# Performance work log

Measured on AMD Instinct MI355X. Metric: run time of the kernel, lower is better.

## Reference

```python
import jax, jax.numpy as jnp
import numpy as np

N = 16384
K = 10
NODE_IN, RF_IN, TXP_IN = 8, 64, 64
EMB = 64            # node_output_dim = rf_output_dim = txp_output_dim
HID = 128           # hidden_dim (fusion output)
DGC = 64            # dgcn_dim
NUM_CLS = 16        # num_node_classes


def _linear_params(key, fan_in, fan_out):
    kw, kb = jax.random.split(key)
    lim = 1.0 / np.sqrt(fan_in)
    W = jax.random.uniform(kw, (fan_in, fan_out), minval=-lim, maxval=lim, dtype=jnp.float32)
    b = jax.random.uniform(kb, (fan_out,), minval=-lim, maxval=lim, dtype=jnp.float32)
    return W, b


def setup_inputs() -> dict:
    key = jax.random.key(0)
    ks = jax.random.split(key, 12)
    node_feat = jax.random.normal(ks[0], (N, NODE_IN), dtype=jnp.float32)
    rf_feat = jax.random.normal(ks[1], (N, RF_IN), dtype=jnp.float32)
    txp_feat = jax.random.normal(ks[2], (N, TXP_IN), dtype=jnp.float32)
    Wb, bb = _linear_params(ks[3], NODE_IN, EMB)
    Wr, br = _linear_params(ks[4], RF_IN, EMB)
    Wt, bt = _linear_params(ks[5], TXP_IN, EMB)
    Wf, bf = _linear_params(ks[6], 3 * EMB, HID)
    We1, be1 = _linear_params(ks[7], 2 * HID, DGC)   # EdgeConv 1 MLP
    We2, be2 = _linear_params(ks[8], 2 * DGC, DGC)   # EdgeConv 2 MLP
    Wc, bc = _linear_params(ks[9], 2 * DGC, NUM_CLS)  # node classifier on concat of both conv outputs
    return {"node_feat": node_feat, "rf_feat": rf_feat, "txp_feat": txp_feat,
            "Wb": Wb, "bb": bb, "Wr": Wr, "br": br, "Wt": Wt, "bt": bt,
            "Wf": Wf, "bf": bf, "We1": We1, "be1": be1, "We2": We2, "be2": be2,
            "Wc": Wc, "bc": bc}


def _knn_idx(x, k):
    # pairwise squared euclidean distances, exclude self, k nearest
    sq = jnp.sum(x * x, axis=1)                      # [N]
    d = sq[:, None] + sq[None, :] - 2.0 * (x @ x.T)  # [N, N]
    n = x.shape[0]
    d = d.at[jnp.arange(n), jnp.arange(n)].set(jnp.inf)
    _, idx = jax.lax.top_k(-d, k)                    # [N, k]
    return idx


def _edge_conv(x, W, b, k):
    # dynamic KNN graph + EdgeConv: max_j leaky_relu(MLP([x_i, x_j - x_i]))
    idx = _knn_idx(x, k)                             # [N, k] int
    xj = x[idx]                                      # [N, k, d]  irregular gather
    xi = jnp.broadcast_to(x[:, None, :], xj.shape)
    e = jnp.concatenate([xi, xj - xi], axis=-1)      # [N, k, 2d]
    h = jax.nn.leaky_relu(jnp.einsum('nke,eo->nko', e, W) + b)
    return jnp.max(h, axis=1)                        # [N, out] max aggregation


def reference(node_feat, rf_feat, txp_feat, Wb, bb, Wr, br, Wt, bt,
              Wf, bf, We1, be1, We2, be2, Wc, bc):
    # per-modality embeds (Linear + ReLU)
    xb = jax.nn.relu(node_feat @ Wb + bb)
    xr = jax.nn.relu(rf_feat @ Wr + br)
    xt = jax.nn.relu(txp_feat @ Wt + bt)
    # fusion (Linear + LeakyReLU)
    h = jax.nn.leaky_relu(jnp.concatenate([xb, xr, xt], axis=-1) @ Wf + bf)  # [N, HID]
    # two dynamic-graph conv (DGC) layers with per-layer KNN
    g1 = _edge_conv(h, We1, be1, K)    # [N, DGC]
    g2 = _edge_conv(g1, We2, be2, K)   # [N, DGC]
    # node classifier on concatenated conv outputs
    logits = jnp.concatenate([g1, g2], axis=-1) @ Wc + bc  # [N, NUM_CLS]
    return logits
```

## Files before the change

### kernel.cpp

```cpp
#include <hip/hip_runtime.h>
#include <hip/hip_bf16.h>

#define N_NODES 16384
#define KNBR 10

__device__ __forceinline__ void gload_lds16(const float* g, void* l) {
    __builtin_amdgcn_global_load_lds((const __attribute__((address_space(1))) void*)g,
                                     (__attribute__((address_space(3))) void*)l,
                                     16, 0, 0);
}

__global__ __launch_bounds__(256) void embed_kernel(
        const float* __restrict__ nf, const float* __restrict__ rf,
        const float* __restrict__ tf,
        const float* __restrict__ Wb, const float* __restrict__ bb,
        const float* __restrict__ Wr, const float* __restrict__ br,
        const float* __restrict__ Wt, const float* __restrict__ bt,
        float* __restrict__ xcat, int n) {
    int t = blockIdx.x * blockDim.x + threadIdx.x;
    if (t >= n * 192) return;
    int i = t / 192, o = t % 192;
    float acc;
    if (o < 64) {
        acc = bb[o];
        #pragma unroll
        for (int d = 0; d < 8; ++d) acc = fmaf(nf[i * 8 + d], Wb[d * 64 + o], acc);
    } else if (o < 128) {
        int oo = o - 64;
        acc = br[oo];
        #pragma unroll 8
        for (int d = 0; d < 64; ++d) acc = fmaf(rf[i * 64 + d], Wr[d * 64 + oo], acc);
    } else {
        int oo = o - 128;
        acc = bt[oo];
        #pragma unroll 8
        for (int d = 0; d < 64; ++d) acc = fmaf(tf[i * 64 + d], Wt[d * 64 + oo], acc);
    }
    xcat[t] = fmaxf(acc, 0.0f);
}

__global__ __launch_bounds__(256) void fuse_kernel(
        const float* __restrict__ xcat, const float* __restrict__ Wf,
        const float* __restrict__ bf, float* __restrict__ h, int n) {
    int t = blockIdx.x * blockDim.x + threadIdx.x;
    if (t >= n * 128) return;
    int i = t >> 7, o = t & 127;
    float acc = bf[o];
    const float* xr = xcat + (size_t)i * 192;
    #pragma unroll 8
    for (int d = 0; d < 192; ++d) acc = fmaf(xr[d], Wf[d * 128 + o], acc);
    h[t] = acc > 0.f ? acc : 0.01f * acc;
}

__global__ void sqnorm_kernel(const float* __restrict__ x, float* __restrict__ sq,
                              int n, int D) {
    int w = (blockIdx.x * blockDim.x + threadIdx.x) >> 6;
    int lane = threadIdx.x & 63;
    if (w >= n) return;
    float s = 0.f;
    for (int d = lane; d < D; d += 64) {
        float v = x[(size_t)w * D + d];
        s = fmaf(v, v, s);
    }
    #pragma unroll
    for (int off = 32; off > 0; off >>= 1) s += __shfl_down(s, off);
    if (lane == 0) sq[w] = s;
}

template <int D>
__global__ __launch_bounds__(256, 2) void knn_kernel(const float* __restrict__ x,
                                                     const float* __restrict__ sq,
                                                     float* __restrict__ pd,
                                                     int* __restrict__ pi, int n) {
    constexpr int TM = 128, TJ = 128, KC = 32, LD4 = KC / 4;
    constexpr int NCH = D / KC;
    constexpr int PSL = 8;

    __shared__ __align__(16) char smem[TM * 65 * 4 + TJ * 4];
    float4* XiC = (float4*)smem;
    float4* XjC = ((float4*)smem) + TM * LD4;
    float*  Dt  = (float*)smem;
    float*  sqj = (float*)(smem + TM * 65 * 4);

    const int tid  = threadIdx.x;
    const int wv   = tid >> 6;
    const int lane = tid & 63;
    const int ty = tid >> 4, tx = tid & 15;
    const int mb = blockIdx.x >> 3, ps = blockIdx.x & 7;
    const int i0 = mb * TM;
    const int jsl = n >> 3;
    const int j0 = ps * jsl;

    int rowS[4], colS[4];
    #pragma unroll
    for (int w = 0; w < 4; ++w) {
        int fi = (wv * 4 + w) * 64 + lane;
        rowS[w] = fi >> 3;
        colS[w] = (fi & 7) ^ (rowS[w] & 7);
    }

    float bd[KNBR];
    int bi[KNBR];
    #pragma unroll
    for (int q = 0; q < KNBR; ++q) { bd[q] = 3.4e38f; bi[q] = 0; }
    const float my_sqi = (tid < TM) ? sq[i0 + tid] : 0.f;

    for (int jt = 0; jt < jsl; jt += TJ) {
        float acc[8][8];
        #pragma unroll
        for (int r = 0; r < 8; ++r)
            #pragma unroll
            for (int c = 0; c < 8; ++c) acc[r][c] = 0.f;

        for (int s = 0; s < NCH; ++s) {
            __syncthreads();
            #pragma unroll
            for (int w = 0; w < 4; ++w)
                gload_lds16(x + (size_t)(i0 + rowS[w]) * D + s * KC + colS[w] * 4,
                            XiC + (wv * 4 + w) * 64);
            #pragma unroll
            for (int w = 0; w < 4; ++w)
                gload_lds16(x + (size_t)(j0 + jt + rowS[w]) * D + s * KC + colS[w] * 4,
                            XjC + (wv * 4 + w) * 64);
            if (s == 0 && tid < TJ) sqj[tid] = sq[j0 + jt + tid];
            __syncthreads();

            #pragma unroll
            for (int d4 = 0; d4 < LD4; ++d4) {
                const int si = d4 ^ (ty & 7);
                const int sj = d4 ^ (tx & 7);
                float4 av[8];
                #pragma unroll
                for (int r = 0; r < 8; ++r) av[r] = XiC[(ty + 16 * r) * LD4 + si];
                #pragma unroll
                for (int c = 0; c < 8; ++c) {
                    float4 bv = XjC[(tx + 16 * c) * LD4 + sj];
                    #pragma unroll
                    for (int r = 0; r < 8; ++r) {
                        acc[r][c] = fmaf(av[r].x, bv.x, acc[r][c]);
                        acc[r][c] = fmaf(av[r].y, bv.y, acc[r][c]);
                        acc[r][c] = fmaf(av[r].z, bv.z, acc[r][c]);
                        acc[r][c] = fmaf(av[r].w, bv.w, acc[r][c]);
                    }
                }
            }
        }

        #pragma unroll
        for (int h = 0; h < 2; ++h) {
            __syncthreads();
            #pragma unroll
            for (int r = 0; r < 8; ++r)
                #pragma unroll
                for (int c = 0; c < 4; ++c)
                    Dt[(ty + 16 * r) * 65 + tx + 16 * c] = acc[r][4 * h + c];
            __syncthreads();
            if (tid < TM) {
                const int ig = i0 + tid;
                const float* drow = Dt + tid * 65;
                const int jb = j0 + jt + 64 * h;
                for (int c2 = 0; c2 < 64; ++c2) {
                    int j = jb + c2;
                    float dist = my_sqi + sqj[64 * h + c2] - 2.0f * drow[c2];
                    if (dist < bd[KNBR - 1] && j != ig) {
                        bd[KNBR - 1] = dist;
                        bi[KNBR - 1] = j;
                        #pragma unroll
                        for (int q2 = KNBR - 2; q2 >= 0; --q2) {
                            if (bd[q2 + 1] < bd[q2]) {
                                float td = bd[q2]; bd[q2] = bd[q2 + 1]; bd[q2 + 1] = td;
                                int tj = bi[q2]; bi[q2] = bi[q2 + 1]; bi[q2 + 1] = tj;
                            }
                        }
                    }
                }
            }
        }
    }

    if (tid < TM) {
        size_t base = ((size_t)(i0 + tid) * PSL + ps) * KNBR;
        #pragma unroll
        for (int q = 0; q < KNBR; ++q) { pd[base + q] = bd[q]; pi[base + q] = bi[q]; }
    }
}

__global__ __launch_bounds__(256) void knn_merge_kernel(const float* __restrict__ pd,
                                                        const int* __restrict__ pi,
                                                        int* __restrict__ idx, int n) {
    int row = blockIdx.x * blockDim.x + threadIdx.x;
    if (row >= n) return;
    float bd[KNBR];
    int bi[KNBR];
    #pragma unroll
    for (int q = 0; q < KNBR; ++q) { bd[q] = 3.4e38f; bi[q] = 0; }
    const float* prow = pd + (size_t)row * 8 * KNBR;
    const int*   irow = pi + (size_t)row * 8 * KNBR;
    for (int e = 0; e < 8 * KNBR; ++e) {
        float dist = prow[e];
        if (dist < bd[KNBR - 1]) {
            bd[KNBR - 1] = dist;
            bi[KNBR - 1] = irow[e];
            #pragma unroll
            for (int q2 = KNBR - 2; q2 >= 0; --q2) {
                if (bd[q2 + 1] < bd[q2]) {
                    float td = bd[q2]; bd[q2] = bd[q2 + 1]; bd[q2 + 1] = td;
                    int tj = bi[q2]; bi[q2] = bi[q2 + 1]; bi[q2 + 1] = tj;
                }
            }
        }
    }
    #pragma unroll
    for (int q = 0; q < KNBR; ++q) idx[(size_t)row * KNBR + q] = bi[q];
}

template <int D>
__global__ __launch_bounds__(64) void edgeconv_kernel(const float* __restrict__ x,
                                                      const int* __restrict__ idx,
                                                      const float* __restrict__ W,
                                                      const float* __restrict__ bias,
                                                      float* __restrict__ out, int n) {
    constexpr int NN = 4;
    constexpr int D4 = D / 4;
    const int base = blockIdx.x * NN;
    const int o = threadIdx.x;

    __shared__ float4 xi4[NN][D4];
    __shared__ float4 xd4[NN][KNBR][D4];
    float* xi = (float*)xi4;
    float* xd = (float*)xd4;

    for (int nn = 0; nn < NN; ++nn)
        for (int d = o; d < D; d += 64) xi[nn * D + d] = x[(size_t)(base + nn) * D + d];
    __syncthreads();
    for (int nn = 0; nn < NN; ++nn)
        for (int k = 0; k < KNBR; ++k) {
            int j = idx[(size_t)(base + nn) * KNBR + k];
            for (int d = o; d < D; d += 64)
                xd[(nn * KNBR + k) * D + d] = x[(size_t)j * D + d] - xi[nn * D + d];
        }
    __syncthreads();

    float a[NN];
    float bo = bias[o];
    #pragma unroll
    for (int nn = 0; nn < NN; ++nn) a[nn] = bo;
    for (int d4 = 0; d4 < D4; ++d4) {
        float4 xv[NN];
        #pragma unroll
        for (int nn = 0; nn < NN; ++nn) xv[nn] = xi4[nn][d4];
        #pragma unroll
        for (int e = 0; e < 4; ++e) {
            float w = W[(d4 * 4 + e) * 64 + o];
            #pragma unroll
            for (int nn = 0; nn < NN; ++nn)
                a[nn] = fmaf(((const float*)&xv[nn])[e], w, a[nn]);
        }
    }

    float m[NN];
    #pragma unroll
    for (int nn = 0; nn < NN; ++nn) m[nn] = -3.4e38f;
    for (int k = 0; k < KNBR; ++k) {
        float acc[NN];
        #pragma unroll
        for (int nn = 0; nn < NN; ++nn) acc[nn] = a[nn];
        for (int d4 = 0; d4 < D4; ++d4) {
            float4 xv[NN];
            #pragma unroll
            for (int nn = 0; nn < NN; ++nn) xv[nn] = xd4[nn][k][d4];
            #pragma unroll
            for (int e = 0; e < 4; ++e) {
                float w = W[(D + d4 * 4 + e) * 64 + o];
                #pragma unroll
                for (int nn = 0; nn < NN; ++nn)
                    acc[nn] = fmaf(((const float*)&xv[nn])[e], w, acc[nn]);
            }
        }
        #pragma unroll
        for (int nn = 0; nn < NN; ++nn) {
            float v = acc[nn] > 0.f ? acc[nn] : 0.01f * acc[nn];
            m[nn] = fmaxf(m[nn], v);
        }
    }
    for (int nn = 0; nn < NN; ++nn) out[(size_t)(base + nn) * 64 + o] = m[nn];
}

__global__ void classifier_kernel(const float* __restrict__ g1, const float* __restrict__ g2,
                                  const float* __restrict__ Wc, const float* __restrict__ bc,
                                  float* __restrict__ out, int n) {
    int t = blockIdx.x * blockDim.x + threadIdx.x;
    if (t >= n * 16) return;
    int i = t >> 4, c = t & 15;
    float acc = bc[c];
    #pragma unroll 8
    for (int d = 0; d < 64; ++d) acc = fmaf(g1[(size_t)i * 64 + d], Wc[d * 16 + c], acc);
    #pragma unroll 8
    for (int d = 0; d < 64; ++d) acc = fmaf(g2[(size_t)i * 64 + d], Wc[(64 + d) * 16 + c], acc);
    out[t] = acc;
}

extern "C" void kernel_launch(void* const* d_in, const int* in_sizes, int n_in,
                              void* d_out, int out_size, void* d_ws, size_t ws_size,
                              hipStream_t stream) {
    const int n = N_NODES;
    const float* node_feat = (const float*)d_in[0];
    const float* rf_feat   = (const float*)d_in[1];
    const float* txp_feat  = (const float*)d_in[2];
    const float* Wb = (const float*)d_in[3];
    const float* bb = (const float*)d_in[4];
    const float* Wr = (const float*)d_in[5];
    const float* br = (const float*)d_in[6];
    const float* Wt = (const float*)d_in[7];
    const float* bt = (const float*)d_in[8];
    const float* Wf = (const float*)d_in[9];
    const float* bf = (const float*)d_in[10];
    const float* We1 = (const float*)d_in[11];
    const float* be1 = (const float*)d_in[12];
    const float* We2 = (const float*)d_in[13];
    const float* be2 = (const float*)d_in[14];
    const float* Wc = (const float*)d_in[15];
    const float* bc = (const float*)d_in[16];

    float* xcat = (float*)d_ws;
    float* h    = xcat + (size_t)n * 192;
    float* sqv  = h + (size_t)n * 128;
    float* g1   = sqv + n;
    float* g2   = g1 + (size_t)n * 64;
    int*   idx  = (int*)(g2 + (size_t)n * 64);
    float* pd   = xcat;
    int*   pi   = (int*)(xcat + (size_t)n * 80);

    embed_kernel<<<(n * 192 + 255) / 256, 256, 0, stream>>>(
        node_feat, rf_feat, txp_feat, Wb, bb, Wr, br, Wt, bt, xcat, n);
    fuse_kernel<<<(n * 128 + 255) / 256, 256, 0, stream>>>(xcat, Wf, bf, h, n);

    sqnorm_kernel<<<(n * 64 + 255) / 256, 256, 0, stream>>>(h, sqv, n, 128);
    knn_kernel<128><<<(n / 128) * 8, 256, 0, stream>>>(h, sqv, pd, pi, n);
    knn_merge_kernel<<<(n + 255) / 256, 256, 0, stream>>>(pd, pi, idx, n);
    edgeconv_kernel<128><<<n / 4, 64, 0, stream>>>(h, idx, We1, be1, g1, n);

    sqnorm_kernel<<<(n * 64 + 255) / 256, 256, 0, stream>>>(g1, sqv, n, 64);
    knn_kernel<64><<<(n / 128) * 8, 256, 0, stream>>>(g1, sqv, pd, pi, n);
    knn_merge_kernel<<<(n + 255) / 256, 256, 0, stream>>>(pd, pi, idx, n);
    edgeconv_kernel<64><<<n / 4, 64, 0, stream>>>(g1, idx, We2, be2, g2, n);

    classifier_kernel<<<(n * 16 + 255) / 256, 256, 0, stream>>>(g1, g2, Wc, bc,
                                                                (float*)d_out, n);
}
```

Before: 3.387 ms.

## Widen KNN distance tile to 256 columns and restructure edgeconv to one node per wave

The KNN kernel now computes a 128x256 distance tile per j-iteration, so each thread holds an 8x16 accumulator. Each loaded i-chunk is reused across twice as many j rows, and global offsets are precomputed. The edgeconv kernel changes from one 64-thread block handling four nodes serially to a 256-thread block where each wave owns one node, with vectorized float4 gathers. Risks are higher register pressure in KNN against the (256,2) launch bound, and per-thread weight loads now reused across one node instead of four.

```diff
diff --git a/kernel.cpp b/kernel.cpp
--- a/kernel.cpp
+++ b/kernel.cpp
@@ -72,15 +72,15 @@
                                                      const float* __restrict__ sq,
                                                      float* __restrict__ pd,
                                                      int* __restrict__ pi, int n) {
-    constexpr int TM = 128, TJ = 128, KC = 32, LD4 = KC / 4;
+    constexpr int TM = 128, TJ = 256, KC = 32, LD4 = KC / 4;
     constexpr int NCH = D / KC;
     constexpr int PSL = 8;
 
-    __shared__ __align__(16) char smem[TM * 65 * 4 + TJ * 4];
+    __shared__ __align__(16) char smem[49152 + 1024];
     float4* XiC = (float4*)smem;
     float4* XjC = ((float4*)smem) + TM * LD4;
     float*  Dt  = (float*)smem;
-    float*  sqj = (float*)(smem + TM * 65 * 4);
+    float*  sqj = (float*)(smem + 49152);
 
     const int tid  = threadIdx.x;
     const int wv   = tid >> 6;
@@ -91,12 +91,18 @@
     const int jsl = n >> 3;
     const int j0 = ps * jsl;
 
-    int rowS[4], colS[4];
+    int offI[4], offJ[8];
     #pragma unroll
     for (int w = 0; w < 4; ++w) {
         int fi = (wv * 4 + w) * 64 + lane;
-        rowS[w] = fi >> 3;
-        colS[w] = (fi & 7) ^ (rowS[w] & 7);
+        int row = fi >> 3, col = (fi & 7) ^ (row & 7);
+        offI[w] = (i0 + row) * D + col * 4;
+    }
+    #pragma unroll
+    for (int w = 0; w < 8; ++w) {
+        int fi = (wv * 8 + w) * 64 + lane;
+        int row = fi >> 3, col = (fi & 7) ^ (row & 7);
+        offJ[w] = (j0 + row) * D + col * 4;
     }
 
     float bd[KNBR];
@@ -106,26 +112,24 @@
     const float my_sqi = (tid < TM) ? sq[i0 + tid] : 0.f;
 
     for (int jt = 0; jt < jsl; jt += TJ) {
-        float acc[8][8];
+        float acc[8][16];
         #pragma unroll
         for (int r = 0; r < 8; ++r)
             #pragma unroll
-            for (int c = 0; c < 8; ++c) acc[r][c] = 0.f;
+            for (int c = 0; c < 16; ++c) acc[r][c] = 0.f;
 
         for (int s = 0; s < NCH; ++s) {
             __syncthreads();
             #pragma unroll
             for (int w = 0; w < 4; ++w)
-                gload_lds16(x + (size_t)(i0 + rowS[w]) * D + s * KC + colS[w] * 4,
-                            XiC + (wv * 4 + w) * 64);
-            #pragma unroll
-            for (int w = 0; w < 4; ++w)
-                gload_lds16(x + (size_t)(j0 + jt + rowS[w]) * D + s * KC + colS[w] * 4,
-                            XjC + (wv * 4 + w) * 64);
-            if (s == 0 && tid < TJ) sqj[tid] = sq[j0 + jt + tid];
+                gload_lds16(x + offI[w] + s * KC, XiC + (wv * 4 + w) * 64);
+            #pragma unroll
+            for (int w = 0; w < 8; ++w)
+                gload_lds16(x + offJ[w] + jt * D + s * KC, XjC + (wv * 8 + w) * 64);
+            if (s == 0) sqj[tid] = sq[j0 + jt + tid];
             __syncthreads();
 
-            #pragma unroll
+            #pragma unroll 2
             for (int d4 = 0; d4 < LD4; ++d4) {
                 const int si = d4 ^ (ty & 7);
                 const int sj = d4 ^ (tx & 7);
@@ -133,7 +137,7 @@
                 #pragma unroll
                 for (int r = 0; r < 8; ++r) av[r] = XiC[(ty + 16 * r) * LD4 + si];
                 #pragma unroll
-                for (int c = 0; c < 8; ++c) {
+                for (int c = 0; c < 16; ++c) {
                     float4 bv = XjC[(tx + 16 * c) * LD4 + sj];
                     #pragma unroll
                     for (int r = 0; r < 8; ++r) {
@@ -147,13 +151,13 @@
         }
 
         #pragma unroll
-        for (int h = 0; h < 2; ++h) {
+        for (int h = 0; h < 4; ++h) {
             __syncthreads();
             #pragma unroll
             for (int r = 0; r < 8; ++r)
                 #pragma unroll
-                for (int c = 0; c < 4; ++c)
-                    Dt[(ty + 16 * r) * 65 + tx + 16 * c] = acc[r][4 * h + c];
+                for (int cc = 0; cc < 4; ++cc)
+                    Dt[(ty + 16 * r) * 65 + tx + 16 * cc] = acc[r][4 * h + cc];
             __syncthreads();
             if (tid < TM) {
                 const int ig = i0 + tid;
@@ -215,75 +219,57 @@
 }
 
 template <int D>
-__global__ __launch_bounds__(64) void edgeconv_kernel(const float* __restrict__ x,
-                                                      const int* __restrict__ idx,
-                                                      const float* __restrict__ W,
-                                                      const float* __restrict__ bias,
-                                                      float* __restrict__ out, int n) {
-    constexpr int NN = 4;
+__global__ __launch_bounds__(256) void edgeconv_kernel(const float* __restrict__ x,
+                                                       const int* __restrict__ idx,
+                                                       const float* __restrict__ W,
+                                                       const float* __restrict__ bias,
+                                                       float* __restrict__ out, int n) {
     constexpr int D4 = D / 4;
-    const int base = blockIdx.x * NN;
-    const int o = threadIdx.x;
-
-    __shared__ float4 xi4[NN][D4];
-    __shared__ float4 xd4[NN][KNBR][D4];
-    float* xi = (float*)xi4;
-    float* xd = (float*)xd4;
-
-    for (int nn = 0; nn < NN; ++nn)
-        for (int d = o; d < D; d += 64) xi[nn * D + d] = x[(size_t)(base + nn) * D + d];
+    const int wv = threadIdx.x >> 6;
+    const int o  = threadIdx.x & 63;
+    const int node = blockIdx.x * 4 + wv;
+
+    __shared__ float4 xi4[4][D4];
+    __shared__ float4 xd4[4][KNBR][D4];
+
+    float4 xif = make_float4(0.f, 0.f, 0.f, 0.f);
+    if (o < D4) {
+        xif = *reinterpret_cast<const float4*>(x + (size_t)node * D + o * 4);
+        xi4[wv][o] = xif;
+    }
+    for (int k = 0; k < KNBR; ++k) {
+        int j = idx[(size_t)node * KNBR + k];
+        if (o < D4) {
+            float4 xj = *reinterpret_cast<const float4*>(x + (size_t)j * D + o * 4);
+            xd4[wv][k][o] = make_float4(xj.x - xif.x, xj.y - xif.y,
+                                        xj.z - xif.z, xj.w - xif.w);
+        }
+    }
     __syncthreads();
-    for (int nn = 0; nn < NN; ++nn)
-        for (int k = 0; k < KNBR; ++k) {
-            int j = idx[(size_t)(base + nn) * KNBR + k];
-            for (int d = o; d < D; d += 64)
-                xd[(nn * KNBR + k) * D + d] = x[(size_t)j * D + d] - xi[nn * D + d];
-        }
-    __syncthreads();
-
-    float a[NN];
-    float bo = bias[o];
-    #pragma unroll
-    for (int nn = 0; nn < NN; ++nn) a[nn] = bo;
+
+    float a = bias[o];
     for (int d4 = 0; d4 < D4; ++d4) {
-        float4 xv[NN];
-        #pragma unroll
-        for (int nn = 0; nn < NN; ++nn) xv[nn] = xi4[nn][d4];
-        #pragma unroll
-        for (int e = 0; e < 4; ++e) {
-            float w = W[(d4 * 4 + e) * 64 + o];
-            #pragma unroll
-            for (int nn = 0; nn < NN; ++nn)
-                a[nn] = fmaf(((const float*)&xv[nn])[e], w, a[nn]);
-        }
-    }
-
-    float m[NN];
-    #pragma unroll
-    for (int nn = 0; nn < NN; ++nn) m[nn] = -3.4e38f;
+        float4 xv = xi4[wv][d4];
+        a = fmaf(xv.x, W[(d4 * 4 + 0) * 64 + o], a);
+        a = fmaf(xv.y, W[(d4 * 4 + 1) * 64 + o], a);
+        a = fmaf(xv.z, W[(d4 * 4 + 2) * 64 + o], a);
+        a = fmaf(xv.w, W[(d4 * 4 + 3) * 64 + o], a);
+    }
+
+    float m = -3.4e38f;
     for (int k = 0; k < KNBR; ++k) {
-        float acc[NN];
-        #pragma unroll
-        for (int nn = 0; nn < NN; ++nn) acc[nn] = a[nn];
+        float acc = a;
         for (int d4 = 0; d4 < D4; ++d4) {
-            float4 xv[NN];
-            #pragma unroll
-            for (int nn = 0; nn < NN; ++nn) xv[nn] = xd4[nn][k][d4];
-            #pragma unroll
-            for (int e = 0; e < 4; ++e) {
-                float w = W[(D + d4 * 4 + e) * 64 + o];
-                #pragma unroll
-                for (int nn = 0; nn < NN; ++nn)
-                    acc[nn] = fmaf(((const float*)&xv[nn])[e], w, acc[nn]);
-            }
-        }
-        #pragma unroll
-        for (int nn = 0; nn < NN; ++nn) {
-            float v = acc[nn] > 0.f ? acc[nn] : 0.01f * acc[nn];
-            m[nn] = fmaxf(m[nn], v);
-        }
-    }
-    for (int nn = 0; nn < NN; ++nn) out[(size_t)(base + nn) * 64 + o] = m[nn];
+            float4 xv = xd4[wv][k][d4];
+            acc = fmaf(xv.x, W[(D + d4 * 4 + 0) * 64 + o], acc);
+            acc = fmaf(xv.y, W[(D + d4 * 4 + 1) * 64 + o], acc);
+            acc = fmaf(xv.z, W[(D + d4 * 4 + 2) * 64 + o], acc);
+            acc = fmaf(xv.w, W[(D + d4 * 4 + 3) * 64 + o], acc);
+        }
+        float v = acc > 0.f ? acc : 0.01f * acc;
+        m = fmaxf(m, v);
+    }
+    out[(size_t)node * 64 + o] = m;
 }
 
 __global__ void classifier_kernel(const float* __restrict__ g1, const float* __restrict__ g2,
@@ -338,12 +324,12 @@
     sqnorm_kernel<<<(n * 64 + 255) / 256, 256, 0, stream>>>(h, sqv, n, 128);
     knn_kernel<128><<<(n / 128) * 8, 256, 0, stream>>>(h, sqv, pd, pi, n);
     knn_merge_kernel<<<(n + 255) / 256, 256, 0, stream>>>(pd, pi, idx, n);
-    edgeconv_kernel<128><<<n / 4, 64, 0, stream>>>(h, idx, We1, be1, g1, n);
+    edgeconv_kernel<128><<<n / 4, 256, 0, stream>>>(h, idx, We1, be1, g1, n);
 
     sqnorm_kernel<<<(n * 64 + 255) / 256, 256, 0, stream>>>(g1, sqv, n, 64);
     knn_kernel<64><<<(n / 128) * 8, 256, 0, stream>>>(g1, sqv, pd, pi, n);
     knn_merge_kernel<<<(n + 255) / 256, 256, 0, stream>>>(pd, pi, idx, n);
-    edgeconv_kernel<64><<<n / 4, 64, 0, stream>>>(g1, idx, We2, be2, g2, n);
+    edgeconv_kernel<64><<<n / 4, 256, 0, stream>>>(g1, idx, We2, be2, g2, n);
 
     classifier_kernel<<<(n * 16 + 255) / 256, 256, 0, stream>>>(g1, g2, Wc, bc,
                                                                 (float*)d_out, n);
```

After: 3.079 ms. -9.1%, faster.
